# Kernel optimization log

Hardware: AMD Instinct MI355X
Metric: run time of the kernel (lower is better)

## Reference

```python
import jax, jax.numpy as jnp
import numpy as np

N = 20000
E = 320000
NEG_SLOPE = 0.2
LN_EPS = 1e-5


def gat_conv(x, W, a_src, a_dst, b, src, dst, heads, ch, concat):
    # x: [N, F_in]; W: [F_in, H*C]; a_src/a_dst: [H, C]; b: [H*C] or [C]
    xl = (x @ W).reshape(N, heads, ch)                      # [N,H,C]
    alpha_src = jnp.sum(xl * a_src, axis=-1)                # [N,H]
    alpha_dst = jnp.sum(xl * a_dst, axis=-1)                # [N,H]
    e = alpha_src[src] + alpha_dst[dst]                     # [E',H]
    e = jax.nn.leaky_relu(e, NEG_SLOPE)
    # segment softmax over incoming edges of each dst node
    m = jax.ops.segment_max(e, dst, num_segments=N)         # [N,H]
    m = jnp.where(jnp.isfinite(m), m, 0.0)
    ex = jnp.exp(e - m[dst])
    denom = jax.ops.segment_sum(ex, dst, num_segments=N)    # [N,H]
    alpha = ex / (denom[dst] + 1e-16)                       # [E',H]
    msg = alpha[:, :, None] * xl[src]                       # [E',H,C]
    out = jax.ops.segment_sum(msg, dst, num_segments=N)     # [N,H,C]
    if concat:
        return out.reshape(N, heads * ch) + b
    return out.mean(axis=1) + b


def layer_norm(x, g, b):
    mu = jnp.mean(x, axis=-1, keepdims=True)
    var = jnp.mean(jnp.square(x - mu), axis=-1, keepdims=True)
    return (x - mu) * jax.lax.rsqrt(var + LN_EPS) * g + b


def setup_inputs() -> dict:
    key = jax.random.key(0)
    ks = jax.random.split(key, 24)
    d = {}
    d["x"] = jax.random.normal(ks[0], (N, 50), dtype=jnp.float32)
    d["edge_index"] = jax.random.randint(ks[1], (2, E), 0, N, dtype=jnp.int64)

    def glorot(k, shape):
        fan = shape[0] + shape[-1]
        return jax.random.normal(k, shape, dtype=jnp.float32) * np.sqrt(2.0 / fan)

    # conv1: 50 -> 256, heads=4, concat
    d["W1"] = glorot(ks[2], (50, 4 * 256))
    d["a_src1"] = glorot(ks[3], (4, 256))
    d["a_dst1"] = glorot(ks[4], (4, 256))
    d["b1"] = jnp.zeros((4 * 256,), jnp.float32)
    # conv2: 1024 -> 256, heads=4, concat
    d["W2"] = glorot(ks[5], (1024, 4 * 256))
    d["a_src2"] = glorot(ks[6], (4, 256))
    d["a_dst2"] = glorot(ks[7], (4, 256))
    d["b2"] = jnp.zeros((4 * 256,), jnp.float32)
    # conv3: 1024 -> 121, heads=6, concat=False
    d["W3"] = glorot(ks[8], (1024, 6 * 121))
    d["a_src3"] = glorot(ks[9], (6, 121))
    d["a_dst3"] = glorot(ks[10], (6, 121))
    d["b3"] = jnp.zeros((121,), jnp.float32)
    # skips
    d["skipW1"] = glorot(ks[11], (50, 1024))
    d["skipb1"] = jnp.zeros((1024,), jnp.float32)
    d["skipW2"] = glorot(ks[12], (1024, 1024))
    d["skipb2"] = jnp.zeros((1024,), jnp.float32)
    # layer norms
    d["g1"] = jnp.ones((1024,), jnp.float32)
    d["beta1"] = jnp.zeros((1024,), jnp.float32)
    d["g2"] = jnp.ones((1024,), jnp.float32)
    d["beta2"] = jnp.zeros((1024,), jnp.float32)
    return d


def reference(x, edge_index, W1, a_src1, a_dst1, b1, W2, a_src2, a_dst2, b2,
              W3, a_src3, a_dst3, b3, skipW1, skipb1, skipW2, skipb2,
              g1, beta1, g2, beta2):
    # add self loops (PyG GATConv default)
    loop = jnp.arange(N, dtype=edge_index.dtype)
    src = jnp.concatenate([edge_index[0], loop])
    dst = jnp.concatenate([edge_index[1], loop])

    h = gat_conv(x, W1, a_src1, a_dst1, b1, src, dst, 4, 256, True)
    h = jax.nn.elu(layer_norm(h + (x @ skipW1 + skipb1), g1, beta1))
    h2 = gat_conv(h, W2, a_src2, a_dst2, b2, src, dst, 4, 256, True)
    h2 = jax.nn.elu(layer_norm(h2 + (h @ skipW2 + skipb2), g2, beta2))
    out = gat_conv(h2, W3, a_src3, a_dst3, b3, src, dst, 6, 121, False)
    return out
```

## Files before the change

### kernel.cpp

```cpp
#include <hip/hip_runtime.h>
#include <hip/hip_bf16.h>
#include <math.h>

typedef __attribute__((ext_vector_type(8))) __bf16 bf16x8;
typedef __attribute__((ext_vector_type(4))) float f32x4;

#if __has_builtin(__builtin_amdgcn_global_load_lds)
#define GLD16(g, l)                                                                      \
    __builtin_amdgcn_global_load_lds(                                                    \
        (const __attribute__((address_space(1))) unsigned int*)(g),                      \
        (__attribute__((address_space(3))) unsigned int*)(l), 16, 0, 0)
#else
#define GLD16(g, l) (*(bf16x8*)(l) = *(const bf16x8*)(g))
#endif

#define GEMM_BODY(A, Bt, K, STORE)                                                       \
    __shared__ __bf16 As[128 * 32];                                                      \
    __shared__ __bf16 Bs[128 * 32];                                                      \
    const int t = threadIdx.x;                                                           \
    const int lane = t & 63;                                                             \
    const int wid = t >> 6;                                                              \
    const int wm = (wid >> 1) << 6;                                                      \
    const int wn = (wid & 1) << 6;                                                       \
    const int bm = blockIdx.y * 128;                                                     \
    const int bn = blockIdx.x * 128;                                                     \
    const int srow = (wid << 4) + (lane >> 2);                                           \
    const int scol = (lane & 3) << 3;                                                    \
    f32x4 acc[4][4];                                                                     \
    _Pragma("unroll") for (int i = 0; i < 4; i++)                                        \
        _Pragma("unroll") for (int j = 0; j < 4; j++)                                    \
            acc[i][j] = (f32x4){0.f, 0.f, 0.f, 0.f};                                     \
    const int m16 = lane & 15;                                                           \
    const int k8 = (lane >> 4) << 3;                                                     \
    for (int k0 = 0; k0 < K; k0 += 32) {                                                 \
        __syncthreads();                                                                 \
        GLD16(A + (size_t)(bm + srow) * K + k0 + scol, As + srow * 32 + scol);           \
        GLD16(A + (size_t)(bm + 64 + srow) * K + k0 + scol, As + (64 + srow) * 32 + scol);\
        GLD16(Bt + (size_t)(bn + srow) * K + k0 + scol, Bs + srow * 32 + scol);          \
        GLD16(Bt + (size_t)(bn + 64 + srow) * K + k0 + scol, Bs + (64 + srow) * 32 + scol);\
        __syncthreads();                                                                 \
        bf16x8 af[4], bfr[4];                                                            \
        _Pragma("unroll") for (int i = 0; i < 4; i++) {                                  \
            af[i] = *(const bf16x8*)(As + (wm + 16 * i + m16) * 32 + k8);                \
            bfr[i] = *(const bf16x8*)(Bs + (wn + 16 * i + m16) * 32 + k8);               \
        }                                                                                \
        _Pragma("unroll") for (int i = 0; i < 4; i++)                                    \
            _Pragma("unroll") for (int j = 0; j < 4; j++)                                \
                acc[i][j] = __builtin_amdgcn_mfma_f32_16x16x32_bf16(af[i], bfr[j],       \
                                                                    acc[i][j], 0, 0, 0); \
    }                                                                                    \
    const int r4 = (lane >> 4) << 2;                                                     \
    STORE

__global__ __launch_bounds__(256) void gemm_bt(const __bf16* __restrict__ A,
                                               const __bf16* __restrict__ Bt,
                                               __bf16* __restrict__ C,
                                               int M, int N, int K) {
    GEMM_BODY(A, Bt, K,
        _Pragma("unroll") for (int i = 0; i < 4; i++)
            _Pragma("unroll") for (int j = 0; j < 4; j++) {
                int col = bn + wn + 16 * j + m16;
                _Pragma("unroll") for (int r = 0; r < 4; r++) {
                    int row = bm + wm + 16 * i + r4 + r;
                    C[(size_t)row * N + col] = (__bf16)acc[i][j][r];
                }
            })
}

__global__ __launch_bounds__(256) void gemm_bt2(const __bf16* __restrict__ A,
                                                const __bf16* __restrict__ Bt,
                                                __bf16* __restrict__ C0,
                                                __bf16* __restrict__ C1,
                                                int M, int K) {
    GEMM_BODY(A, Bt, K,
        __bf16* Cp = (bn < 1024) ? C0 : C1;
        const int cb = bn & 1023;
        _Pragma("unroll") for (int i = 0; i < 4; i++)
            _Pragma("unroll") for (int j = 0; j < 4; j++) {
                int col = cb + wn + 16 * j + m16;
                _Pragma("unroll") for (int r = 0; r < 4; r++) {
                    int row = bm + wm + 16 * i + r4 + r;
                    Cp[(size_t)row * 1024 + col] = (__bf16)acc[i][j][r];
                }
            })
}

__device__ __forceinline__ void transpose_tile(const float* __restrict__ W,
                                               __bf16* __restrict__ WT,
                                               int K, int N, int Kp, int Np,
                                               int bx, int by, float* sm) {
    int tx = threadIdx.x & 31, ty = threadIdx.x >> 5;
#pragma unroll
    for (int r = ty; r < 32; r += 8) {
        int k = by * 32 + r, n = bx * 32 + tx;
        float v = 0.f;
        if (k < K && n < N) v = W[(size_t)k * N + n];
        sm[r * 33 + tx] = v;
    }
    __syncthreads();
#pragma unroll
    for (int r = ty; r < 32; r += 8) {
        int n = bx * 32 + r, k = by * 32 + tx;
        if (n < Np && k < Kp) WT[(size_t)n * Kp + k] = (__bf16)sm[tx * 33 + r];
    }
}

__device__ __forceinline__ void transpose_w3_tile(const float* __restrict__ W,
                                                  __bf16* __restrict__ WT,
                                                  int bx, int by, float* sm) {
    int tx = threadIdx.x & 31, ty = threadIdx.x >> 5;
    int r0 = bx * 32;
    int h = r0 >> 7;
    int c0 = r0 & 127;
#pragma unroll
    for (int r = ty; r < 32; r += 8) {
        int k = by * 32 + r;
        int c = c0 + tx;
        float v = 0.f;
        if (c < 121) v = W[(size_t)k * 726 + h * 121 + c];
        sm[r * 33 + tx] = v;
    }
    __syncthreads();
#pragma unroll
    for (int r = ty; r < 32; r += 8) {
        int rr = r0 + r;
        int k = by * 32 + tx;
        WT[(size_t)rr * 1024 + k] = (__bf16)sm[tx * 33 + r];
    }
}

__global__ __launch_bounds__(256) void prep_k(const float* __restrict__ x,
                                              const float* __restrict__ W1,
                                              const float* __restrict__ sW1,
                                              const float* __restrict__ W2,
                                              const float* __restrict__ sW2,
                                              const float* __restrict__ W3,
                                              __bf16* __restrict__ xp,
                                              __bf16* __restrict__ WTcat1,
                                              __bf16* __restrict__ WTcat2,
                                              __bf16* __restrict__ W3pT, int Nn) {
    __shared__ float sm[32 * 33];
    int b = blockIdx.x;
    if (b < 5024) {
        int i = b * 256 + threadIdx.x;
        int n = i >> 6, c = i & 63;
        float v = 0.f;
        if (n < Nn && c < 50) v = x[n * 50 + c];
        xp[(size_t)n * 64 + c] = (__bf16)v;
    } else if (b < 5088) {
        int i = b - 5024; transpose_tile(W1, WTcat1, 50, 1024, 64, 1024, i % 32, i / 32, sm);
    } else if (b < 5152) {
        int i = b - 5088; transpose_tile(sW1, WTcat1 + 1024 * 64, 50, 1024, 64, 1024, i % 32, i / 32, sm);
    } else if (b < 6176) {
        int i = b - 5152; transpose_tile(W2, WTcat2, 1024, 1024, 1024, 1024, i % 32, i / 32, sm);
    } else if (b < 7200) {
        int i = b - 6176; transpose_tile(sW2, WTcat2 + (size_t)1024 * 1024, 1024, 1024, 1024, 1024, i % 32, i / 32, sm);
    } else {
        int i = b - 7200; transpose_w3_tile(W3, W3pT, i % 24, i / 24, sm);
    }
}

__global__ void zero_probe_k(const int* __restrict__ ei, int* __restrict__ cnt,
                             int* __restrict__ flag, int Nn) {
    int i = blockIdx.x * 256 + threadIdx.x;
    if (i < Nn) cnt[i] = 0;
    if (blockIdx.x == 0 && threadIdx.x == 0) {
        int all0 = 1;
        for (int k = 0; k < 64; k++)
            if (ei[2 * k + 1] != 0) { all0 = 0; break; }
        *flag = all0;
    }
}

__device__ __forceinline__ int load_ei(const int* ei, int idx, int is64) {
    return is64 ? ei[2 * idx] : ei[idx];
}

__global__ void hist_k(const int* __restrict__ ei, const int* __restrict__ flag,
                       int* __restrict__ cnt, int E, int Nn) {
    int e = blockIdx.x * 256 + threadIdx.x;
    if (e >= E + Nn) return;
    int is64 = *flag;
    int d = (e < E) ? load_ei(ei, E + e, is64) : (e - E);
    d = min(max(d, 0), Nn - 1);
    atomicAdd(&cnt[d], 1);
}

__global__ __launch_bounds__(1024) void scan_k(int* __restrict__ cnt, int* __restrict__ row_ptr,
                                               int Nn) {
    __shared__ int part[1024];
    int t = threadIdx.x;
    int chunk = (Nn + 1023) >> 10;
    int lo = t * chunk;
    int hi = lo + chunk; if (hi > Nn) hi = Nn; if (lo > Nn) lo = Nn;
    int s = 0;
    for (int i = lo; i < hi; i++) s += (cnt[i] + 7) & ~7;
    part[t] = s;
    __syncthreads();
    for (int off = 1; off < 1024; off <<= 1) {
        int v = (t >= off) ? part[t - off] : 0;
        __syncthreads();
        part[t] += v;
        __syncthreads();
    }
    int run = part[t] - s;
    for (int i = lo; i < hi; i++) { row_ptr[i] = run; run += (cnt[i] + 7) & ~7; }
    if (t == 1023) row_ptr[Nn] = part[1023];
    __syncthreads();
    for (int i = lo; i < hi; i++) cnt[i] = 0;
}

__global__ void fill_csr_k(const int* __restrict__ ei, const int* __restrict__ flag,
                           const int* __restrict__ row_ptr, int* __restrict__ cursor,
                           int* __restrict__ src_csr, int E, int Nn) {
    int e = blockIdx.x * 256 + threadIdx.x;
    if (e >= E + Nn) return;
    int is64 = *flag;
    int d = (e < E) ? load_ei(ei, E + e, is64) : (e - E);
    int s = (e < E) ? load_ei(ei, e, is64) : (e - E);
    d = min(max(d, 0), Nn - 1);
    s = min(max(s, 0), Nn - 1);
    int slot = row_ptr[d] + atomicAdd(&cursor[d], 1);
    src_csr[slot] = s;
}

__global__ void alpha_k(const __bf16* __restrict__ XL, int ld, const float* __restrict__ a_src,
                        const float* __restrict__ a_dst, float* __restrict__ asrc,
                        float* __restrict__ adst, int Nn, int H, int C, int Cpad) {
    int gw = (blockIdx.x * 256 + threadIdx.x) >> 6;
    int lane = threadIdx.x & 63;
    if (gw >= Nn * H) return;
    int n = gw / H, h = gw - n * H;
    const __bf16* row = XL + (size_t)n * ld + h * Cpad;
    const float* as = a_src + h * C;
    const float* ad = a_dst + h * C;
    float s = 0.f, d = 0.f;
    for (int c = lane; c < C; c += 64) {
        float v = (float)row[c];
        s += v * as[c];
        d += v * ad[c];
    }
#pragma unroll
    for (int off = 32; off; off >>= 1) {
        s += __shfl_down(s, off);
        d += __shfl_down(d, off);
    }
    if (lane == 0) { asrc[n * H + h] = s; adst[n * H + h] = d; }
}

__global__ void attn_k(const int* __restrict__ row_ptr, const int* __restrict__ deg,
                       const int* __restrict__ src_csr,
                       const float* __restrict__ asrc, const float* __restrict__ adst,
                       float* __restrict__ wt, int Nn, int H, int Ecap) {
    int gw = (blockIdx.x * 256 + threadIdx.x) >> 6;
    int lane = threadIdx.x & 63;
    if (gw >= Nn) return;
    int n = gw;
    int base = row_ptr[n], dg = deg[n];
    if (dg <= 64) {
        bool v = lane < dg;
        int src = v ? src_csr[base + lane] : 0;
        for (int h = 0; h < H; h++) {
            float ad = adst[n * H + h];
            float e = -1e30f;
            if (v) {
                e = asrc[src * H + h] + ad;
                e = e > 0.f ? e : 0.2f * e;
            }
            float m = e;
#pragma unroll
            for (int off = 1; off < 64; off <<= 1) m = fmaxf(m, __shfl_xor(m, off));
            float ex = v ? __expf(e - m) : 0.f;
            float sum = ex;
#pragma unroll
            for (int off = 1; off < 64; off <<= 1) sum += __shfl_xor(sum, off);
            if (v) wt[(size_t)h * Ecap + base + lane] = ex / (sum + 1e-16f);
        }
        return;
    }
    for (int h = 0; h < H; h++) {
        float ad = adst[n * H + h];
        float m = -1e30f;
        for (int s = lane; s < dg; s += 64) {
            float e = asrc[src_csr[base + s] * H + h] + ad;
            e = e > 0.f ? e : 0.2f * e;
            m = fmaxf(m, e);
        }
#pragma unroll
        for (int off = 1; off < 64; off <<= 1) m = fmaxf(m, __shfl_xor(m, off));
        float sum = 0.f;
        for (int s = lane; s < dg; s += 64) {
            float e = asrc[src_csr[base + s] * H + h] + ad;
            e = e > 0.f ? e : 0.2f * e;
            sum += __expf(e - m);
        }
#pragma unroll
        for (int off = 1; off < 64; off <<= 1) sum += __shfl_xor(sum, off);
        float inv = 1.f / (sum + 1e-16f);
        float* wrow = wt + (size_t)h * Ecap;
        for (int s = lane; s < dg; s += 64) {
            float e = asrc[src_csr[base + s] * H + h] + ad;
            e = e > 0.f ? e : 0.2f * e;
            wrow[base + s] = __expf(e - m) * inv;
        }
    }
}

__global__ __launch_bounds__(256) void agg_skip8(const __bf16* __restrict__ XL,
                                                 const float* __restrict__ wt,
                                                 const int* __restrict__ row_ptr,
                                                 const int* __restrict__ src_csr,
                                                 const float* __restrict__ bias,
                                                 const float* __restrict__ sb,
                                                 __bf16* __restrict__ SK, int Nn, int Ecap) {
    const int cc = blockIdx.x;
    const int n = blockIdx.y * 4 + (threadIdx.x >> 6);
    const int lane = threadIdx.x & 63;
    if (n >= Nn) return;
    const int g = lane >> 4;
    const int p = lane & 15;
    const int col = cc * 128 + p * 8;
    const float* wrow = wt + (size_t)(cc >> 1) * Ecap;
    const __bf16* XLc = XL + col;
    const int base = row_ptr[n], end = row_ptr[n + 1];

    float acc[8];
#pragma unroll
    for (int j = 0; j < 8; j++) acc[j] = 0.f;

    for (int e = base; e < end; e += 8) {
        int2 si = *(const int2*)(src_csr + e + 2 * g);
        float2 wv = *(const float2*)(wrow + e + 2 * g);
        bf16x8 xa = *(const bf16x8*)(XLc + (size_t)si.x * 1024);
        bf16x8 xb = *(const bf16x8*)(XLc + (size_t)si.y * 1024);
#pragma unroll
        for (int j = 0; j < 8; j++) acc[j] += wv.x * (float)xa[j] + wv.y * (float)xb[j];
    }
#pragma unroll
    for (int j = 0; j < 8; j++) {
        acc[j] += __shfl_xor(acc[j], 16);
        acc[j] += __shfl_xor(acc[j], 32);
    }
    if (lane < 16) {
        size_t o = (size_t)n * 1024 + col;
        bf16x8 sk = *(const bf16x8*)(SK + o);
        bf16x8 res;
#pragma unroll
        for (int j = 0; j < 8; j++)
            res[j] = (__bf16)(acc[j] + bias[col + j] + sb[col + j] + (float)sk[j]);
        *(bf16x8*)(SK + o) = res;
    }
}

__global__ __launch_bounds__(256) void agg_mean8(const __bf16* __restrict__ XL,
                                                 const float* __restrict__ wt,
                                                 const int* __restrict__ row_ptr,
                                                 const int* __restrict__ src_csr,
                                                 __bf16* __restrict__ part, int Nn, int Ecap) {
    const int cc = blockIdx.x;
    const int n = blockIdx.y * 4 + (threadIdx.x >> 6);
    const int lane = threadIdx.x & 63;
    if (n >= Nn) return;
    const int g = lane >> 4;
    const int p = lane & 15;
    const int col = cc * 128 + p * 8;
    const float* wrow = wt + (size_t)cc * Ecap;
    const __bf16* XLc = XL + col;
    const int base = row_ptr[n], end = row_ptr[n + 1];

    float acc[8];
#pragma unroll
    for (int j = 0; j < 8; j++) acc[j] = 0.f;

    for (int e = base; e < end; e += 8) {
        int2 si = *(const int2*)(src_csr + e + 2 * g);
        float2 wv = *(const float2*)(wrow + e + 2 * g);
        bf16x8 xa = *(const bf16x8*)(XLc + (size_t)si.x * 768);
        bf16x8 xb = *(const bf16x8*)(XLc + (size_t)si.y * 768);
#pragma unroll
        for (int j = 0; j < 8; j++) acc[j] += wv.x * (float)xa[j] + wv.y * (float)xb[j];
    }
#pragma unroll
    for (int j = 0; j < 8; j++) {
        acc[j] += __shfl_xor(acc[j], 16);
        acc[j] += __shfl_xor(acc[j], 32);
    }
    if (lane < 16) {
        size_t o = (size_t)n * 768 + col;
        bf16x8 res;
#pragma unroll
        for (int j = 0; j < 8; j++) res[j] = (__bf16)acc[j];
        *(bf16x8*)(part + o) = res;
    }
}

__global__ __launch_bounds__(128) void reduce_mean_k(const __bf16* __restrict__ part,
                                                     const float* __restrict__ b3,
                                                     float* __restrict__ out, int Nn) {
    int n = blockIdx.x;
    int t = threadIdx.x;
    if (t >= 121) return;
    const __bf16* row = part + (size_t)n * 768;
    float s = 0.f;
#pragma unroll
    for (int h = 0; h < 6; h++) s += (float)row[h * 128 + t];
    out[(size_t)n * 121 + t] = s * (1.f / 6.f) + b3[t];
}

__global__ __launch_bounds__(256) void ln_elu_k(const __bf16* __restrict__ in,
                                                const float* __restrict__ g,
                                                const float* __restrict__ be,
                                                __bf16* __restrict__ out, int rows_real) {
    const int D = 1024;
    int n = blockIdx.x;
    int t = threadIdx.x;
    size_t ro = (size_t)n * D;
    if (n >= rows_real) {
#pragma unroll
        for (int j = 0; j < 4; j++) out[ro + t + 256 * j] = (__bf16)0.f;
        return;
    }
    float v[4];
    float s = 0.f, q = 0.f;
#pragma unroll
    for (int j = 0; j < 4; j++) {
        int c = t + 256 * j;
        float a = (float)in[ro + c];
        v[j] = a;
        s += a;
        q += a * a;
    }
#pragma unroll
    for (int off = 32; off; off >>= 1) {
        s += __shfl_down(s, off);
        q += __shfl_down(q, off);
    }
    __shared__ float rs[8];
    int wid = t >> 6;
    if ((t & 63) == 0) { rs[wid] = s; rs[wid + 4] = q; }
    __syncthreads();
    s = rs[0] + rs[1] + rs[2] + rs[3];
    q = rs[4] + rs[5] + rs[6] + rs[7];
    float mu = s * (1.f / 1024.f);
    float var = q * (1.f / 1024.f) - mu * mu;
    float inv = rsqrtf(fmaxf(var, 0.f) + 1e-5f);
#pragma unroll
    for (int j = 0; j < 4; j++) {
        int c = t + 256 * j;
        float y = (v[j] - mu) * inv * g[c] + be[c];
        y = y > 0.f ? y : expm1f(y);
        out[ro + c] = (__bf16)y;
    }
}

extern "C" void kernel_launch(void* const* d_in, const int* in_sizes, int n_in,
                              void* d_out, int out_size, void* d_ws, size_t ws_size,
                              hipStream_t stream) {
    const float* x   = (const float*)d_in[0];
    const int*   ei  = (const int*)d_in[1];
    const float* W1  = (const float*)d_in[2];
    const float* as1 = (const float*)d_in[3];
    const float* ad1 = (const float*)d_in[4];
    const float* b1  = (const float*)d_in[5];
    const float* W2  = (const float*)d_in[6];
    const float* as2 = (const float*)d_in[7];
    const float* ad2 = (const float*)d_in[8];
    const float* b2  = (const float*)d_in[9];
    const float* W3  = (const float*)d_in[10];
    const float* as3 = (const float*)d_in[11];
    const float* ad3 = (const float*)d_in[12];
    const float* b3  = (const float*)d_in[13];
    const float* sW1 = (const float*)d_in[14];
    const float* sb1 = (const float*)d_in[15];
    const float* sW2 = (const float*)d_in[16];
    const float* sb2 = (const float*)d_in[17];
    const float* g1  = (const float*)d_in[18];
    const float* be1 = (const float*)d_in[19];
    const float* g2  = (const float*)d_in[20];
    const float* be2 = (const float*)d_in[21];
    float* out = (float*)d_out;

    const int Nn = 20000;
    const int E = in_sizes[1] / 2;
    const int E2 = E + Nn;
    const int Ecap = E2 + 8 * Nn;
    const int Mpad = 20096;

    char* p = (char*)d_ws;
    auto alloc = [&](size_t bytes) {
        char* r = p;
        p += (bytes + 255) & ~(size_t)255;
        return r;
    };
    __bf16* WTcat1 = (__bf16*)alloc((size_t)2048 * 64 * 2);
    __bf16* WTcat2 = (__bf16*)alloc((size_t)2048 * 1024 * 2);
    __bf16* W3pT   = (__bf16*)alloc((size_t)768 * 1024 * 2);
    __bf16* xp     = (__bf16*)alloc((size_t)Mpad * 64 * 2);
    __bf16* XL     = (__bf16*)alloc((size_t)Mpad * 1024 * 2);
    __bf16* SK     = (__bf16*)alloc((size_t)Mpad * 1024 * 2);
    __bf16* H1     = (__bf16*)alloc((size_t)Mpad * 1024 * 2);
    float*  asrcb  = (float*)alloc((size_t)Nn * 6 * 4);
    float*  adstb  = (float*)alloc((size_t)Nn * 6 * 4);
    float*  wbuf   = (float*)alloc((size_t)6 * Ecap * 4);
    int*    rowp   = (int*)alloc((size_t)(Nn + 1) * 4);
    int*    cnt    = (int*)alloc((size_t)Nn * 4);
    int*    scsr   = (int*)alloc((size_t)Ecap * 4);
    int*    eiflag = (int*)alloc(256);
    __bf16* part   = SK;
    (void)ws_size; (void)n_in; (void)out_size;

    prep_k<<<7968, 256, 0, stream>>>(x, W1, sW1, W2, sW2, W3, xp, WTcat1, WTcat2, W3pT, Nn);

    zero_probe_k<<<(Nn + 255) / 256, 256, 0, stream>>>(ei, cnt, eiflag, Nn);
    hist_k<<<(E2 + 255) / 256, 256, 0, stream>>>(ei, eiflag, cnt, E, Nn);
    scan_k<<<1, 1024, 0, stream>>>(cnt, rowp, Nn);
    (void)hipMemsetAsync(scsr, 0, (size_t)Ecap * 4, stream);
    (void)hipMemsetAsync(wbuf, 0, (size_t)6 * Ecap * 4, stream);
    fill_csr_k<<<(E2 + 255) / 256, 256, 0, stream>>>(ei, eiflag, rowp, cnt, scsr, E, Nn);

    gemm_bt2<<<dim3(16, Mpad / 128), 256, 0, stream>>>(xp, WTcat1, XL, SK, Mpad, 64);
    alpha_k<<<(Nn * 4 * 64) / 256, 256, 0, stream>>>(XL, 1024, as1, ad1, asrcb, adstb, Nn, 4, 256, 256);
    attn_k<<<(Nn + 3) / 4, 256, 0, stream>>>(rowp, cnt, scsr, asrcb, adstb, wbuf, Nn, 4, Ecap);
    agg_skip8<<<dim3(8, (Nn + 3) / 4), 256, 0, stream>>>(XL, wbuf, rowp, scsr, b1, sb1, SK, Nn, Ecap);
    ln_elu_k<<<Mpad, 256, 0, stream>>>(SK, g1, be1, H1, Nn);

    gemm_bt2<<<dim3(16, Mpad / 128), 256, 0, stream>>>(H1, WTcat2, XL, SK, Mpad, 1024);
    alpha_k<<<(Nn * 4 * 64) / 256, 256, 0, stream>>>(XL, 1024, as2, ad2, asrcb, adstb, Nn, 4, 256, 256);
    attn_k<<<(Nn + 3) / 4, 256, 0, stream>>>(rowp, cnt, scsr, asrcb, adstb, wbuf, Nn, 4, Ecap);
    agg_skip8<<<dim3(8, (Nn + 3) / 4), 256, 0, stream>>>(XL, wbuf, rowp, scsr, b2, sb2, SK, Nn, Ecap);
    ln_elu_k<<<Mpad, 256, 0, stream>>>(SK, g2, be2, H1, Nn);

    gemm_bt<<<dim3(6, Mpad / 128), 256, 0, stream>>>(H1, W3pT, XL, Mpad, 768, 1024);
    alpha_k<<<(Nn * 6 * 64) / 256, 256, 0, stream>>>(XL, 768, as3, ad3, asrcb, adstb, Nn, 6, 121, 128);
    attn_k<<<(Nn + 3) / 4, 256, 0, stream>>>(rowp, cnt, scsr, asrcb, adstb, wbuf, Nn, 6, Ecap);
    agg_mean8<<<dim3(6, (Nn + 3) / 4), 256, 0, stream>>>(XL, wbuf, rowp, scsr, part, Nn, Ecap);
    reduce_mean_k<<<Nn, 128, 0, stream>>>(part, b3, out, Nn);
}
```

Baseline: 782.5 us.

## Replace 128x128 GEMM with double-buffered 256x256 tile kernel and XCD swizzle

The bf16 MFMA GEMMs move from 128x128 tiles with a single LDS buffer to 256x256 tiles run by 512 threads. Each step covers K=64, with double-buffered global-to-LDS loads interleaved with half-step MFMA batches, explicit vmcnt waits and setprio. Workgroup IDs are remapped so neighbouring tiles land on the same XCD, and padded M grows to a multiple of 256, which also shifts the prep kernel's block ranges. The aim is more data reuse and overlap of loads with compute, at the cost of 128KB LDS per block and heavy register pressure. For the K=64 layer-1 GEMM, a single K iteration leaves little to pipeline.

```diff
diff --git a/kernel.cpp b/kernel.cpp
--- a/kernel.cpp
+++ b/kernel.cpp
@@ -14,75 +14,142 @@
 #define GLD16(g, l) (*(bf16x8*)(l) = *(const bf16x8*)(g))
 #endif
 
-#define GEMM_BODY(A, Bt, K, STORE)                                                       \
-    __shared__ __bf16 As[128 * 32];                                                      \
-    __shared__ __bf16 Bs[128 * 32];                                                      \
-    const int t = threadIdx.x;                                                           \
-    const int lane = t & 63;                                                             \
-    const int wid = t >> 6;                                                              \
-    const int wm = (wid >> 1) << 6;                                                      \
-    const int wn = (wid & 1) << 6;                                                       \
-    const int bm = blockIdx.y * 128;                                                     \
-    const int bn = blockIdx.x * 128;                                                     \
-    const int srow = (wid << 4) + (lane >> 2);                                           \
-    const int scol = (lane & 3) << 3;                                                    \
-    f32x4 acc[4][4];                                                                     \
-    _Pragma("unroll") for (int i = 0; i < 4; i++)                                        \
+#define BAR() asm volatile("s_barrier" ::: "memory")
+#define WAITVM(N) asm volatile("s_waitcnt vmcnt(" #N ")" ::: "memory")
+
+
+#define STAGE_H(Base, regidx, t_, kh_)                                                   \
+    do {                                                                                 \
+        __bf16* Ld = lds + ((((t_) & 1) * 4 + (regidx)) * 8192);                         \
+        const __bf16* Gp = (Base) + (t_) * 64 + (kh_) * 32;                              \
+        GLD16(Gp, Ld + tt * 8);                                                          \
+        GLD16(Gp + (size_t)128 * K_, Ld + (tt + 512) * 8);                               \
+    } while (0)
+
+#define LOAD_A(t_, kh_)                                                                  \
+    {                                                                                    \
+        const __bf16* Ar = lds + (((t_) & 1) * 4 + (kh_)) * 8192 + aoff;                 \
+        _Pragma("unroll") for (int i = 0; i < 8; i++)                                    \
+            af[i] = *(const bf16x8*)(Ar + i * 512);                                      \
+    }
+
+#define LOAD_B2(t_, kh_, j0)                                                             \
+    {                                                                                    \
+        const __bf16* Br = lds + (((t_) & 1) * 4 + 2 + (kh_)) * 8192 + boff;             \
+        _Pragma("unroll") for (int j = 0; j < 2; j++)                                    \
+            bf[(j0) + j] = *(const bf16x8*)(Br + ((j0) + j) * 512);                      \
+    }
+
+#define MFMA_HALF(j0)                                                                    \
+    __builtin_amdgcn_s_setprio(1);                                                       \
+    _Pragma("unroll") for (int i = 0; i < 8; i++)                                        \
+        _Pragma("unroll") for (int j = (j0); j < (j0) + 2; j++)                          \
+            acc[i][j] = __builtin_amdgcn_mfma_f32_16x16x32_bf16(af[i], bf[j],            \
+                                                                acc[i][j], 0, 0, 0);     \
+    __builtin_amdgcn_s_setprio(0);
+
+#define GEMM256_BODY(A, Bt, K_, STORE)                                                   \
+    __shared__ __align__(16) __bf16 lds[65536];                                          \
+    const int tt = threadIdx.x;                                                          \
+    const int lane = tt & 63;                                                            \
+    const int wid = tt >> 6;                                                             \
+    const int wr = wid >> 2;                                           \
+    const int wc = wid & 3;                                         \
+     \
+    const int nwg = gridDim.x * gridDim.y;                                               \
+    const int wg0 = blockIdx.y * gridDim.x + blockIdx.x;                                 \
+    const int qq = nwg >> 3, rr = nwg & 7, xcd = wg0 & 7, oo = wg0 >> 3;                 \
+    const int swz = (xcd < rr ? xcd * (qq + 1) : rr * (qq + 1) + (xcd - rr) * qq) + oo;  \
+    const int bm = (swz / gridDim.x) * 256;                                              \
+    const int bn = (swz % gridDim.x) * 256;                                              \
+    const int m16 = lane & 15;                                                           \
+    const int c4 = lane >> 4;                                                            \
+    const int NT = K_ >> 6;                                                              \
+    const int srow = tt >> 2;                                                            \
+    const int sch = (tt & 3) << 3;                                                       \
+    const __bf16* Abase = A + (size_t)(bm + srow) * K_ + sch;                            \
+    const __bf16* Bbase = Bt + (size_t)(bn + srow) * K_ + sch;                           \
+    const int aoff = (wr * 128 + m16) * 32 + c4 * 8;                                     \
+    const int boff = (wc * 64 + m16) * 32 + c4 * 8;                                      \
+    f32x4 acc[8][4];                                                                     \
+    _Pragma("unroll") for (int i = 0; i < 8; i++)                                        \
         _Pragma("unroll") for (int j = 0; j < 4; j++)                                    \
             acc[i][j] = (f32x4){0.f, 0.f, 0.f, 0.f};                                     \
-    const int m16 = lane & 15;                                                           \
-    const int k8 = (lane >> 4) << 3;                                                     \
-    for (int k0 = 0; k0 < K; k0 += 32) {                                                 \
-        __syncthreads();                                                                 \
-        GLD16(A + (size_t)(bm + srow) * K + k0 + scol, As + srow * 32 + scol);           \
-        GLD16(A + (size_t)(bm + 64 + srow) * K + k0 + scol, As + (64 + srow) * 32 + scol);\
-        GLD16(Bt + (size_t)(bn + srow) * K + k0 + scol, Bs + srow * 32 + scol);          \
-        GLD16(Bt + (size_t)(bn + 64 + srow) * K + k0 + scol, Bs + (64 + srow) * 32 + scol);\
-        __syncthreads();                                                                 \
-        bf16x8 af[4], bfr[4];                                                            \
-        _Pragma("unroll") for (int i = 0; i < 4; i++) {                                  \
-            af[i] = *(const bf16x8*)(As + (wm + 16 * i + m16) * 32 + k8);                \
-            bfr[i] = *(const bf16x8*)(Bs + (wn + 16 * i + m16) * 32 + k8);               \
-        }                                                                                \
-        _Pragma("unroll") for (int i = 0; i < 4; i++)                                    \
-            _Pragma("unroll") for (int j = 0; j < 4; j++)                                \
-                acc[i][j] = __builtin_amdgcn_mfma_f32_16x16x32_bf16(af[i], bfr[j],       \
-                                                                    acc[i][j], 0, 0, 0); \
+    bf16x8 af[8], bf[4];                                                                 \
+     \
+    STAGE_H(Abase, 0, 0, 0);                                                             \
+    STAGE_H(Bbase, 2, 0, 0);                                                             \
+    STAGE_H(Abase, 1, 0, 1);                                                             \
+    STAGE_H(Bbase, 3, 0, 1);                                                             \
+    WAITVM(4);                                                                           \
+    BAR();                                                                               \
+    for (int t = 0; t < NT; t++) {                                                       \
+        const bool pre = (t + 1 < NT);                                                   \
+                                                                                 \
+        LOAD_A(t, 0);                                                                    \
+        LOAD_B2(t, 0, 0);                                                                \
+        if (pre) STAGE_H(Abase, 0, t + 1, 0);                                            \
+        BAR();                                                                           \
+        MFMA_HALF(0);                                                                    \
+        BAR();                                                                           \
+                                                                                 \
+        LOAD_B2(t, 0, 2);                                                                \
+        if (pre) STAGE_H(Bbase, 2, t + 1, 0);                                            \
+        BAR();                                                                           \
+        MFMA_HALF(2);                                                                    \
+        if (pre) { WAITVM(4); } else { WAITVM(0); }                                      \
+        BAR();                                                                           \
+                                                                                 \
+        LOAD_A(t, 1);                                                                    \
+        LOAD_B2(t, 1, 0);                                                                \
+        if (pre) STAGE_H(Abase, 1, t + 1, 1);                                            \
+        BAR();                                                                           \
+        MFMA_HALF(0);                                                                    \
+        BAR();                                                                           \
+                                                                                 \
+        LOAD_B2(t, 1, 2);                                                                \
+        if (pre) STAGE_H(Bbase, 3, t + 1, 1);                                            \
+        BAR();                                                                           \
+        MFMA_HALF(2);                                                                    \
+        if (pre) { WAITVM(4); }                                                          \
+        BAR();                                                                           \
     }                                                                                    \
-    const int r4 = (lane >> 4) << 2;                                                     \
     STORE
 
-__global__ __launch_bounds__(256) void gemm_bt(const __bf16* __restrict__ A,
-                                               const __bf16* __restrict__ Bt,
-                                               __bf16* __restrict__ C,
-                                               int M, int N, int K) {
-    GEMM_BODY(A, Bt, K,
-        _Pragma("unroll") for (int i = 0; i < 4; i++)
-            _Pragma("unroll") for (int j = 0; j < 4; j++) {
-                int col = bn + wn + 16 * j + m16;
-                _Pragma("unroll") for (int r = 0; r < 4; r++) {
-                    int row = bm + wm + 16 * i + r4 + r;
-                    C[(size_t)row * N + col] = (__bf16)acc[i][j][r];
-                }
-            })
-}
-
-__global__ __launch_bounds__(256) void gemm_bt2(const __bf16* __restrict__ A,
-                                                const __bf16* __restrict__ Bt,
-                                                __bf16* __restrict__ C0,
-                                                __bf16* __restrict__ C1,
-                                                int M, int K) {
-    GEMM_BODY(A, Bt, K,
-        __bf16* Cp = (bn < 1024) ? C0 : C1;
-        const int cb = bn & 1023;
-        _Pragma("unroll") for (int i = 0; i < 4; i++)
-            _Pragma("unroll") for (int j = 0; j < 4; j++) {
-                int col = cb + wn + 16 * j + m16;
-                _Pragma("unroll") for (int r = 0; r < 4; r++) {
-                    int row = bm + wm + 16 * i + r4 + r;
-                    Cp[(size_t)row * 1024 + col] = (__bf16)acc[i][j][r];
-                }
-            })
+__global__ __launch_bounds__(512, 2) void gemm256_bt(const __bf16* __restrict__ A,
+                                                     const __bf16* __restrict__ Bt,
+                                                     __bf16* __restrict__ C,
+                                                     int M, int N_, int K_) {
+    GEMM256_BODY(A, Bt, K_,
+        { const int r4 = c4 << 2;
+          const int rb = bm + wr * 128;
+          const int cb = bn + wc * 64;
+          _Pragma("unroll") for (int i = 0; i < 8; i++)
+              _Pragma("unroll") for (int j = 0; j < 4; j++) {
+                  int col = cb + j * 16 + m16;
+                  size_t rowb = (size_t)(rb + i * 16 + r4) * N_ + col;
+                  _Pragma("unroll") for (int r = 0; r < 4; r++)
+                      C[rowb + (size_t)r * N_] = (__bf16)acc[i][j][r];
+              } })
+}
+
+__global__ __launch_bounds__(512, 2) void gemm256_bt2(const __bf16* __restrict__ A,
+                                                      const __bf16* __restrict__ Bt,
+                                                      __bf16* __restrict__ C0,
+                                                      __bf16* __restrict__ C1,
+                                                      int M, int K_) {
+    GEMM256_BODY(A, Bt, K_,
+        { __bf16* Cp = (bn < 1024) ? C0 : C1;
+          const int r4 = c4 << 2;
+          const int rb = bm + wr * 128;
+          const int cb = (bn & 1023) + wc * 64;
+          _Pragma("unroll") for (int i = 0; i < 8; i++)
+              _Pragma("unroll") for (int j = 0; j < 4; j++) {
+                  int col = cb + j * 16 + m16;
+                  size_t rowb = (size_t)(rb + i * 16 + r4) * 1024 + col;
+                  _Pragma("unroll") for (int r = 0; r < 4; r++)
+                      Cp[rowb + (size_t)r * 1024] = (__bf16)acc[i][j][r];
+              } })
 }
 
 __device__ __forceinline__ void transpose_tile(const float* __restrict__ W,
@@ -141,22 +208,22 @@
                                               __bf16* __restrict__ W3pT, int Nn) {
     __shared__ float sm[32 * 33];
     int b = blockIdx.x;
-    if (b < 5024) {
+    if (b < 5056) {
         int i = b * 256 + threadIdx.x;
         int n = i >> 6, c = i & 63;
         float v = 0.f;
         if (n < Nn && c < 50) v = x[n * 50 + c];
         xp[(size_t)n * 64 + c] = (__bf16)v;
-    } else if (b < 5088) {
-        int i = b - 5024; transpose_tile(W1, WTcat1, 50, 1024, 64, 1024, i % 32, i / 32, sm);
-    } else if (b < 5152) {
-        int i = b - 5088; transpose_tile(sW1, WTcat1 + 1024 * 64, 50, 1024, 64, 1024, i % 32, i / 32, sm);
-    } else if (b < 6176) {
-        int i = b - 5152; transpose_tile(W2, WTcat2, 1024, 1024, 1024, 1024, i % 32, i / 32, sm);
-    } else if (b < 7200) {
-        int i = b - 6176; transpose_tile(sW2, WTcat2 + (size_t)1024 * 1024, 1024, 1024, 1024, 1024, i % 32, i / 32, sm);
+    } else if (b < 5120) {
+        int i = b - 5056; transpose_tile(W1, WTcat1, 50, 1024, 64, 1024, i % 32, i / 32, sm);
+    } else if (b < 5184) {
+        int i = b - 5120; transpose_tile(sW1, WTcat1 + 1024 * 64, 50, 1024, 64, 1024, i % 32, i / 32, sm);
+    } else if (b < 6208) {
+        int i = b - 5184; transpose_tile(W2, WTcat2, 1024, 1024, 1024, 1024, i % 32, i / 32, sm);
+    } else if (b < 7232) {
+        int i = b - 6208; transpose_tile(sW2, WTcat2 + (size_t)1024 * 1024, 1024, 1024, 1024, 1024, i % 32, i / 32, sm);
     } else {
-        int i = b - 7200; transpose_w3_tile(W3, W3pT, i % 24, i / 24, sm);
+        int i = b - 7232; transpose_w3_tile(W3, W3pT, i % 24, i / 24, sm);
     }
 }
 
@@ -484,7 +551,7 @@
     const int E = in_sizes[1] / 2;
     const int E2 = E + Nn;
     const int Ecap = E2 + 8 * Nn;
-    const int Mpad = 20096;
+    const int Mpad = 20224;
 
     char* p = (char*)d_ws;
     auto alloc = [&](size_t bytes) {
@@ -509,7 +576,7 @@
     __bf16* part   = SK;
     (void)ws_size; (void)n_in; (void)out_size;
 
-    prep_k<<<7968, 256, 0, stream>>>(x, W1, sW1, W2, sW2, W3, xp, WTcat1, WTcat2, W3pT, Nn);
+    prep_k<<<8000, 256, 0, stream>>>(x, W1, sW1, W2, sW2, W3, xp, WTcat1, WTcat2, W3pT, Nn);
 
     zero_probe_k<<<(Nn + 255) / 256, 256, 0, stream>>>(ei, cnt, eiflag, Nn);
     hist_k<<<(E2 + 255) / 256, 256, 0, stream>>>(ei, eiflag, cnt, E, Nn);
@@ -518,19 +585,19 @@
     (void)hipMemsetAsync(wbuf, 0, (size_t)6 * Ecap * 4, stream);
     fill_csr_k<<<(E2 + 255) / 256, 256, 0, stream>>>(ei, eiflag, rowp, cnt, scsr, E, Nn);
 
-    gemm_bt2<<<dim3(16, Mpad / 128), 256, 0, stream>>>(xp, WTcat1, XL, SK, Mpad, 64);
+    gemm256_bt2<<<dim3(8, Mpad / 256), 512, 0, stream>>>(xp, WTcat1, XL, SK, Mpad, 64);
     alpha_k<<<(Nn * 4 * 64) / 256, 256, 0, stream>>>(XL, 1024, as1, ad1, asrcb, adstb, Nn, 4, 256, 256);
     attn_k<<<(Nn + 3) / 4, 256, 0, stream>>>(rowp, cnt, scsr, asrcb, adstb, wbuf, Nn, 4, Ecap);
     agg_skip8<<<dim3(8, (Nn + 3) / 4), 256, 0, stream>>>(XL, wbuf, rowp, scsr, b1, sb1, SK, Nn, Ecap);
     ln_elu_k<<<Mpad, 256, 0, stream>>>(SK, g1, be1, H1, Nn);
 
-    gemm_bt2<<<dim3(16, Mpad / 128), 256, 0, stream>>>(H1, WTcat2, XL, SK, Mpad, 1024);
+    gemm256_bt2<<<dim3(8, Mpad / 256), 512, 0, stream>>>(H1, WTcat2, XL, SK, Mpad, 1024);
     alpha_k<<<(Nn * 4 * 64) / 256, 256, 0, stream>>>(XL, 1024, as2, ad2, asrcb, adstb, Nn, 4, 256, 256);
     attn_k<<<(Nn + 3) / 4, 256, 0, stream>>>(rowp, cnt, scsr, asrcb, adstb, wbuf, Nn, 4, Ecap);
     agg_skip8<<<dim3(8, (Nn + 3) / 4), 256, 0, stream>>>(XL, wbuf, rowp, scsr, b2, sb2, SK, Nn, Ecap);
     ln_elu_k<<<Mpad, 256, 0, stream>>>(SK, g2, be2, H1, Nn);
 
-    gemm_bt<<<dim3(6, Mpad / 128), 256, 0, stream>>>(H1, W3pT, XL, Mpad, 768, 1024);
+    gemm256_bt<<<dim3(3, Mpad / 256), 512, 0, stream>>>(H1, W3pT, XL, Mpad, 768, 1024);
     alpha_k<<<(Nn * 6 * 64) / 256, 256, 0, stream>>>(XL, 768, as3, ad3, asrcb, adstb, Nn, 6, 121, 128);
     attn_k<<<(Nn + 3) / 4, 256, 0, stream>>>(rowp, cnt, scsr, asrcb, adstb, wbuf, Nn, 6, Ecap);
     agg_mean8<<<dim3(6, (Nn + 3) / 4), 256, 0, stream>>>(XL, wbuf, rowp, scsr, part, Nn, Ecap);
```

After: 757.0 us. -3.3%, faster.
